# Optimization experiments

Measured on AMD Instinct MI355X. Metric: run time of the kernel, lower is better.

## Reference

```python
import jax, jax.numpy as jnp
import numpy as np
from jax import lax

NEG = -1e30  # log-space 'zero' (avoid -inf for numerical safety)
EPS = 1e-7   # keras.backend.epsilon(), added before log in ctc_batch_cost


def _ctc_loss(y_pred, y_true):
    """CTC negative log-likelihood, full input/label lengths, blank = C-1.

    y_pred: [B, T, C] probabilities (post-softmax, as keras ctc_batch_cost expects)
    y_true: [B, L] int labels in [0, C-2]
    returns [B, 1] loss per example (matches keras ctc_batch_cost output shape)
    """
    B, T, C = y_pred.shape
    L = y_true.shape[1]
    S = 2 * L + 1
    blank = C - 1

    logp = jnp.log(y_pred + EPS)  # [B, T, C]

    # Extended label sequence: blank, l1, blank, l2, ..., lL, blank
    ext = jnp.full((B, S), blank, dtype=y_true.dtype)
    ext = ext.at[:, 1::2].set(y_true)  # [B, S]

    # s-2 skip transition allowed iff ext[s] != blank and ext[s] != ext[s-2]
    allow = jnp.concatenate(
        [jnp.zeros((B, 2), dtype=bool),
         (ext[:, 2:] != blank) & (ext[:, 2:] != ext[:, :-2])], axis=1)  # [B, S]

    # Gather log-probs of extended labels per time step: [T, B, S]
    logp_t = jnp.transpose(logp, (1, 0, 2))  # [T, B, C]
    idx = jnp.broadcast_to(ext[None, :, :], (T, B, S))
    lp_ext = jnp.take_along_axis(logp_t, idx, axis=2)  # [T, B, S]

    # alpha init at t=0: only s=0 (blank) and s=1 (first label) reachable
    alpha0 = jnp.full((B, S), NEG, dtype=logp.dtype)
    alpha0 = alpha0.at[:, 0].set(lp_ext[0, :, 0])
    alpha0 = alpha0.at[:, 1].set(lp_ext[0, :, 1])

    neg1 = jnp.full((B, 1), NEG, dtype=logp.dtype)
    neg2 = jnp.full((B, 2), NEG, dtype=logp.dtype)

    def step(alpha, lp):
        a1 = jnp.concatenate([neg1, alpha[:, :-1]], axis=1)
        a2 = jnp.concatenate([neg2, alpha[:, :-2]], axis=1)
        a = jnp.logaddexp(alpha, a1)
        a = jnp.logaddexp(a, jnp.where(allow, a2, NEG))
        return a + lp, None

    alphaT, _ = lax.scan(step, alpha0, lp_ext[1:])  # sequential over T-1 steps

    loss = -jnp.logaddexp(alphaT[:, S - 1], alphaT[:, S - 2])  # [B]
    return loss[:, None]


def setup_inputs() -> dict:
    key = jax.random.key(0)
    k1, k2 = jax.random.split(key)
    B, T, C, L = 512, 512, 128, 64
    logits = jax.random.normal(k1, (B, T, C), dtype=jnp.float32)
    y_pred = jax.nn.softmax(logits, axis=-1)  # ctc_batch_cost expects probabilities
    y_true = jax.random.randint(k2, (B, L), 0, C - 1)  # labels in [0, C-2]; blank=C-1
    return {"y_true": y_true, "y_pred": y_pred}


def reference(y_true, y_pred):
    return _ctc_loss(y_pred, y_true)
```

## Files before the change

kernel.cpp:

```cpp
#include <hip/hip_runtime.h>
#include <hip/hip_bf16.h>


typedef unsigned int u32;
typedef unsigned long long u64;

constexpr int B = 512, T = 512, C = 128, L = 64;
constexpr int BLANK = C - 1;
constexpr int GR = L + 1;
constexpr int NCHUNK = T / 8;
constexpr float EPS = 1e-7f;
constexpr float NEG = -1e30f;
constexpr float LN2 = 0.69314718055994530942f;

__global__ __launch_bounds__(256)
void gather_kernel(const int* __restrict__ y_true,
                   const float* __restrict__ y_pred,
                   uint4* __restrict__ G2) {
    __shared__ float sp[64 * 128];
    __shared__ int slab[GR];
    const int b   = blockIdx.x >> 3;
    const int t0  = (blockIdx.x & 7) * 64;
    const int tid = threadIdx.x;

    if (tid < GR) slab[tid] = (tid < L) ? y_true[b * L + tid] : BLANK;

    const float4* __restrict__ src4 =
        (const float4*)(y_pred + ((size_t)b * T + t0) * C);
    float4* sp4 = (float4*)sp;
#pragma unroll
    for (int i = 0; i < 8; ++i) sp4[i * 256 + tid] = src4[i * 256 + tid];
    __syncthreads();

#pragma unroll
    for (int it = 0; it < 3; ++it) {
        const int item = it * 256 + tid;
        if (item < 8 * GR) {
            const int chunk = item / GR;
            const int r     = item - chunk * GR;
            const int lab   = slab[r];
            u32 w[4];
#pragma unroll
            for (int q = 0; q < 4; ++q) {
                const float v0 = sp[(chunk * 8 + 2 * q)     * 128 + lab] + EPS;
                const float v1 = sp[(chunk * 8 + 2 * q + 1) * 128 + lab] + EPS;
                u32 b0 = __float_as_uint(v0);
                u32 b1 = __float_as_uint(v1);
                b0 = (b0 + 0x7FFFu + ((b0 >> 16) & 1u)) >> 16;
                b1 = (b1 + 0x7FFFu + ((b1 >> 16) & 1u)) & 0xFFFF0000u;
                w[q] = b0 | b1;
            }
            G2[((size_t)b * NCHUNK + (t0 >> 3) + chunk) * GR + r] =
                make_uint4(w[0], w[1], w[2], w[3]);
        }
    }
}

__device__ __forceinline__ double dpp64_shr1(double x) {
    union { double d; u32 u[2]; } in, out;
    in.d = x;
    out.u[0] = (u32)__builtin_amdgcn_update_dpp(0, (int)in.u[0], 0x138, 0xF, 0xF, false);
    out.u[1] = (u32)__builtin_amdgcn_update_dpp(0, (int)in.u[1], 0x138, 0xF, 0xF, false);
    return out.d;
}
template <int CTRL>
__device__ __forceinline__ u32 dpp_maxu_step(u32 m) {
    u32 t = (u32)__builtin_amdgcn_update_dpp(0, (int)m, CTRL, 0xF, 0xF, false);
    return m > t ? m : t;
}
__device__ __forceinline__ double exp2_exact(int e) {
    union { double d; u64 u; } s; s.u = (u64)(1023 + e) << 52; return s.d;
}

struct Bank { uint4 own[4]; uint4 blk[4]; };

__global__ __launch_bounds__(64, 1)
void scan_kernel(const int* __restrict__ y_true,
                 const uint4* __restrict__ G2,
                 float* __restrict__ out) {
    const int b = blockIdx.x;
    const int l = threadIdx.x;

    const int lab = y_true[b * L + l];
    const int lab_prev = __shfl_up(lab, 1);
    const bool allow1 = (l >= 1) && (lab != lab_prev);

    const uint4* __restrict__ ownB = G2 + (size_t)b * NCHUNK * GR + l;
    const uint4* __restrict__ blkB = G2 + (size_t)b * NCHUNK * GR + L;

    auto load_bank = [&](Bank& bk, int c0) {
#pragma unroll
        for (int c = 0; c < 4; ++c) {
            bk.own[c] = ownB[(c0 + c) * GR];
            bk.blk[c] = blkB[(c0 + c) * GR];
        }
    };

    double d0 = (l == 0) ? 1.0 : 0.0;
    double d1 = 0.0;
    double d2 = 0.0;
    int Ce = 0;

    auto consume_bank = [&](const Bank& bk) {
#pragma unroll
        for (int c = 0; c < 4; ++c) {
            const u32* ow = (const u32*)&bk.own[c];
            const u32* bw = (const u32*)&bk.blk[c];
#pragma unroll
            for (int j = 0; j < 8; ++j) {
                const u32 wo = ow[j >> 1], wb = bw[j >> 1];
                const float fl = __uint_as_float((j & 1) ? (wo & 0xFFFF0000u) : (wo << 16));
                const float fb = __uint_as_float((j & 1) ? (wb & 0xFFFF0000u) : (wb << 16));
                const double Pl = (double)fl, Pb = (double)fb;
                const double p0  = dpp64_shr1(d1);
                const double sel = allow1 ? p0 : 0.0;
                const double nd0 = (d0 + p0) * Pb;
                const double nd2 = (d2 + d1) * Pb;
                const double nd1 = (d1 + (d0 + sel)) * Pl;
                d0 = nd0; d1 = nd1; d2 = nd2;
            }
        }
    };

    auto renorm = [&]() {
        u32 h0 = (u32)__double2hiint(d0);
        u32 h1 = (u32)__double2hiint(d1);
        u32 m = h0 > h1 ? h0 : h1;
        m = dpp_maxu_step<0x111>(m);
        m = dpp_maxu_step<0x112>(m);
        m = dpp_maxu_step<0x114>(m);
        m = dpp_maxu_step<0x118>(m);
        m = dpp_maxu_step<0x142>(m);
        m = dpp_maxu_step<0x143>(m);
        const u32 M = (u32)__builtin_amdgcn_readlane((int)m, 63);
        const int e = (int)((M >> 20) & 0x7FFu) - 1023;
        const double s = exp2_exact(-e);
        d0 *= s; d1 *= s; d2 *= s;
        Ce += e;
    };

    Bank A, Bk;
    load_bank(A, 0);
    load_bank(Bk, 4);

#pragma unroll 1
    for (int k = 0; k < 16; k += 2) {
        consume_bank(A);
        if (k + 2 < 16) load_bank(A, (k + 2) * 4);
        renorm();
        consume_bank(Bk);
        if (k + 3 < 16) load_bank(Bk, (k + 3) * 4);
        renorm();
    }

    if (l == 63) {
        const double sum = d1 + d2;
        const int ee = ((__double2hiint(sum) >> 20) & 0x7FF) - 1023;
        const float mant = (float)(sum * exp2_exact(-ee));
        out[b] = -((float)(Ce + ee) + __log2f(mant)) * LN2;
    }
}

__device__ __forceinline__ float lae2(float x, float y) {
    float m = fmaxf(x, y);
    float d = fminf(x, y) - m;
    return m + __logf(1.0f + __expf(d));
}
__device__ __forceinline__ float lae3(float x, float y, float z) {
    float m = fmaxf(fmaxf(x, y), z);
    float e = __expf(x - m) + __expf(y - m) + __expf(z - m);
    return m + __logf(e);
}
__global__ __launch_bounds__(64)
void ctc_fallback(const int* __restrict__ y_true,
                  const float* __restrict__ y_pred,
                  float* __restrict__ out) {
    const int b = blockIdx.x;
    const int l = threadIdx.x;
    const float* __restrict__ pb = y_pred + (size_t)b * T * C;
    const int lab = y_true[b * L + l];
    const int lab_prev = __shfl_up(lab, 1);
    const bool allow1 = (l >= 1) && (lab != lab_prev);
    float a0, a1, a2;
    {
        float pbl = pb[BLANK];
        float pla = pb[lab];
        a0 = (l == 0) ? __logf(pbl + EPS) : NEG;
        a1 = (l == 0) ? __logf(pla + EPS) : NEG;
        a2 = NEG;
    }
    for (int t = 1; t < T; ++t) {
        const float lpb = __logf(pb[t * C + BLANK] + EPS);
        const float lpl = __logf(pb[t * C + lab] + EPS);
        float p0 = __shfl_up(a1, 1);
        if (l == 0) p0 = NEG;
        const float na0 = lae2(a0, p0) + lpb;
        const float na1 = lae3(a1, a0, allow1 ? p0 : NEG) + lpl;
        const float na2 = lae2(a2, a1) + lpb;
        a0 = na0; a1 = na1; a2 = na2;
    }
    if (l == 63) out[b] = -lae2(a2, a1);
}

extern "C" void kernel_launch(void* const* d_in, const int* in_sizes, int n_in,
                              void* d_out, int out_size, void* d_ws, size_t ws_size,
                              hipStream_t stream) {
    const int*   y_true = (const int*)d_in[0];
    const float* y_pred = (const float*)d_in[1];
    float*       out    = (float*)d_out;

    const size_t need = (size_t)B * NCHUNK * GR * sizeof(uint4);
    if (ws_size >= need) {
        uint4* G2 = (uint4*)d_ws;
        gather_kernel<<<dim3(B * (T / 64)), dim3(256), 0, stream>>>(y_true, y_pred, G2);
        scan_kernel<<<dim3(B), dim3(64), 0, stream>>>(y_true, G2, out);
    } else {
        ctc_fallback<<<dim3(B), dim3(64), 0, stream>>>(y_true, y_pred, out);
    }
}
```

Measured before the change: 213.9 us.

## Rewrite gather as register-resident wave shuffle and split blank/label planes

The gather kernel no longer stages 64x128 tiles in shared memory. Each wave streams float2 rows with double-buffered register loads and uses ds_bpermute to pick each lane's label probability and a shuffle to fetch the blank probability. The workspace is split into a per-lane label plane and a separate compact blank plane, so the scan kernel loads the blank chunk from a contiguous array instead of a strided 65-row layout. This drops LDS traffic and the 65-row indexing in exchange for more cross-lane permute instructions and fewer, larger blocks (1024 of them).

```diff
diff --git a/kernel.cpp b/kernel.cpp
--- a/kernel.cpp
+++ b/kernel.cpp
@@ -7,52 +7,65 @@
 
 constexpr int B = 512, T = 512, C = 128, L = 64;
 constexpr int BLANK = C - 1;
-constexpr int GR = L + 1;
 constexpr int NCHUNK = T / 8;
 constexpr float EPS = 1e-7f;
 constexpr float NEG = -1e30f;
 constexpr float LN2 = 0.69314718055994530942f;
 
+__device__ __forceinline__ u32 rne16(u32 b) {
+    return (b + 0x7FFFu + ((b >> 16) & 1u)) >> 16;
+}
+
 __global__ __launch_bounds__(256)
 void gather_kernel(const int* __restrict__ y_true,
                    const float* __restrict__ y_pred,
-                   uint4* __restrict__ G2) {
-    __shared__ float sp[64 * 128];
-    __shared__ int slab[GR];
-    const int b   = blockIdx.x >> 3;
-    const int t0  = (blockIdx.x & 7) * 64;
-    const int tid = threadIdx.x;
-
-    if (tid < GR) slab[tid] = (tid < L) ? y_true[b * L + tid] : BLANK;
-
-    const float4* __restrict__ src4 =
-        (const float4*)(y_pred + ((size_t)b * T + t0) * C);
-    float4* sp4 = (float4*)sp;
-#pragma unroll
-    for (int i = 0; i < 8; ++i) sp4[i * 256 + tid] = src4[i * 256 + tid];
-    __syncthreads();
-
-#pragma unroll
-    for (int it = 0; it < 3; ++it) {
-        const int item = it * 256 + tid;
-        if (item < 8 * GR) {
-            const int chunk = item / GR;
-            const int r     = item - chunk * GR;
-            const int lab   = slab[r];
-            u32 w[4];
-#pragma unroll
-            for (int q = 0; q < 4; ++q) {
-                const float v0 = sp[(chunk * 8 + 2 * q)     * 128 + lab] + EPS;
-                const float v1 = sp[(chunk * 8 + 2 * q + 1) * 128 + lab] + EPS;
-                u32 b0 = __float_as_uint(v0);
-                u32 b1 = __float_as_uint(v1);
-                b0 = (b0 + 0x7FFFu + ((b0 >> 16) & 1u)) >> 16;
-                b1 = (b1 + 0x7FFFu + ((b1 >> 16) & 1u)) & 0xFFFF0000u;
-                w[q] = b0 | b1;
-            }
-            G2[((size_t)b * NCHUNK + (t0 >> 3) + chunk) * GR + r] =
-                make_uint4(w[0], w[1], w[2], w[3]);
-        }
+                   uint4* __restrict__ G2a,
+                   uint4* __restrict__ G2b) {
+    const int b    = blockIdx.x >> 1;
+    const int half = blockIdx.x & 1;
+    const int wave = threadIdx.x >> 6;
+    const int lane = threadIdx.x & 63;
+
+    const int lab  = y_true[b * L + lane];
+    const int perm = (lab >> 1) << 2;
+    const bool sel_hi = (lab & 1);
+
+    const float2* __restrict__ base =
+        (const float2*)(y_pred + (size_t)b * T * C) + lane;
+    const int c0 = half * 32 + wave * 8;
+
+    float2 buf[2][8];
+#pragma unroll
+    for (int j = 0; j < 8; ++j) buf[0][j] = base[(c0 * 8 + j) * 64];
+
+#pragma unroll
+    for (int i = 0; i < 8; ++i) {
+        const int c = c0 + i;
+        if (i + 1 < 8) {
+#pragma unroll
+            for (int j = 0; j < 8; ++j)
+                buf[(i + 1) & 1][j] = base[((c + 1) * 8 + j) * 64];
+        }
+        const float2* row = buf[i & 1];
+
+        u32 gl[8], gb[8];
+#pragma unroll
+        for (int j = 0; j < 8; ++j) {
+            const int vx = __builtin_amdgcn_ds_bpermute(perm, __float_as_int(row[j].x));
+            const int vy = __builtin_amdgcn_ds_bpermute(perm, __float_as_int(row[j].y));
+            const float v = __int_as_float(sel_hi ? vy : vx) + EPS;
+            gl[j] = __float_as_uint(v);
+            gb[j] = __float_as_uint(__shfl(row[j].y, 63) + EPS);
+        }
+        u32 wl[4], wb[4];
+#pragma unroll
+        for (int q = 0; q < 4; ++q) {
+            wl[q] = rne16(gl[2 * q]) | (rne16(gl[2 * q + 1]) << 16);
+            wb[q] = rne16(gb[2 * q]) | (rne16(gb[2 * q + 1]) << 16);
+        }
+        G2a[(((size_t)b * NCHUNK + c) << 6) + lane] = make_uint4(wl[0], wl[1], wl[2], wl[3]);
+        if (lane == 0)
+            G2b[(size_t)b * NCHUNK + c] = make_uint4(wb[0], wb[1], wb[2], wb[3]);
     }
 }
 
@@ -76,7 +89,8 @@
 
 __global__ __launch_bounds__(64, 1)
 void scan_kernel(const int* __restrict__ y_true,
-                 const uint4* __restrict__ G2,
+                 const uint4* __restrict__ G2a,
+                 const uint4* __restrict__ G2b,
                  float* __restrict__ out) {
     const int b = blockIdx.x;
     const int l = threadIdx.x;
@@ -85,14 +99,14 @@
     const int lab_prev = __shfl_up(lab, 1);
     const bool allow1 = (l >= 1) && (lab != lab_prev);
 
-    const uint4* __restrict__ ownB = G2 + (size_t)b * NCHUNK * GR + l;
-    const uint4* __restrict__ blkB = G2 + (size_t)b * NCHUNK * GR + L;
+    const uint4* __restrict__ ownB = G2a + (((size_t)b * NCHUNK) << 6) + l;
+    const uint4* __restrict__ blkB = G2b + (size_t)b * NCHUNK;
 
     auto load_bank = [&](Bank& bk, int c0) {
 #pragma unroll
         for (int c = 0; c < 4; ++c) {
-            bk.own[c] = ownB[(c0 + c) * GR];
-            bk.blk[c] = blkB[(c0 + c) * GR];
+            bk.own[c] = ownB[(size_t)(c0 + c) << 6];
+            bk.blk[c] = blkB[c0 + c];
         }
     };
 
@@ -209,11 +223,14 @@
     const float* y_pred = (const float*)d_in[1];
     float*       out    = (float*)d_out;
 
-    const size_t need = (size_t)B * NCHUNK * GR * sizeof(uint4);
+    const size_t nA = (size_t)B * NCHUNK * 64;
+    const size_t nB = (size_t)B * NCHUNK;
+    const size_t need = (nA + nB) * sizeof(uint4);
     if (ws_size >= need) {
-        uint4* G2 = (uint4*)d_ws;
-        gather_kernel<<<dim3(B * (T / 64)), dim3(256), 0, stream>>>(y_true, y_pred, G2);
-        scan_kernel<<<dim3(B), dim3(64), 0, stream>>>(y_true, G2, out);
+        uint4* G2a = (uint4*)d_ws;
+        uint4* G2b = G2a + nA;
+        gather_kernel<<<dim3(B * 2), dim3(256), 0, stream>>>(y_true, y_pred, G2a, G2b);
+        scan_kernel<<<dim3(B), dim3(64), 0, stream>>>(y_true, G2a, G2b, out);
     } else {
         ctc_fallback<<<dim3(B), dim3(64), 0, stream>>>(y_true, y_pred, out);
     }
```

Result: no change. 213.0 us (-0.4%).
